# Performance work log

Hardware: AMD Instinct MI355X
Metric: run time of the kernel (lower is better)

## Reference

```python
import jax, jax.numpy as jnp
import numpy as np

LAMBDA_OPACITY = 1e-3
LAMBDA_DIST = 1e-3
LAMBDA_SAM = 1e-4
MIN_PIXNUM = 2
N_RAYS = 65536
S = 48            # samples per ray
NPIX = 65536      # semantic supervised pixels
C = 256           # number of SAM clusters
D = 16            # semantic feature dim


def setup_inputs() -> dict:
    key = jax.random.key(0)
    k = jax.random.split(key, 8)
    rgb_pred = jax.random.normal(k[0], (NPIX, 3), dtype=jnp.float32) * 0.1 + 0.5
    rgb_gt = jax.random.uniform(k[1], (NPIX, 3), dtype=jnp.float32)
    opacity = jax.random.uniform(k[2], (NPIX, 1), dtype=jnp.float32, minval=0.01, maxval=0.99)
    N = N_RAYS * S
    ws = jax.random.uniform(k[3], (N,), dtype=jnp.float32) / S
    deltas = jax.random.uniform(k[4], (N,), dtype=jnp.float32, minval=1e-3, maxval=2e-2)
    # midpoints: sorted (cumsum of deltas) within each ray, as the CUDA scan assumes
    ts = jnp.cumsum(deltas.reshape(N_RAYS, S), axis=1).reshape(N)
    ridx = jnp.arange(N_RAYS, dtype=jnp.int32)
    rays_a = jnp.stack([ridx, ridx * S, jnp.full((N_RAYS,), S, jnp.int32)], axis=1)
    sam = jax.random.randint(k[5], (NPIX, 1), 1, C + 1, dtype=jnp.int32)  # all > 0 (valid)
    semantic = jax.random.normal(k[6], (NPIX, D), dtype=jnp.float32)
    return dict(rgb_pred=rgb_pred, rgb_gt=rgb_gt, opacity=opacity, ws=ws,
                deltas=deltas, ts=ts, rays_a=rays_a, sam=sam, semantic=semantic)


def distortion_loss(ws, deltas, ts, rays_a):
    # Mip-NeRF 360 distortion via per-ray exclusive scans (DVGO-v2 form):
    # loss_ray = sum_i 2*w_i*(t_i*W_{<i} - (wt)_{<i}) + sum_i w_i^2*delta_i/3
    n_rays = rays_a.shape[0]
    starts = rays_a[:, 1]
    N = ws.shape[0]
    ray_ids = jnp.searchsorted(starts, jnp.arange(N, dtype=starts.dtype), side='right') - 1
    w_excl_g = jnp.cumsum(ws) - ws                 # global exclusive scan
    W_excl = w_excl_g - w_excl_g[starts][ray_ids]  # per-ray exclusive scan
    wts = ws * ts
    wt_excl_g = jnp.cumsum(wts) - wts
    WT_excl = wt_excl_g - wt_excl_g[starts][ray_ids]
    per_sample = 2.0 * ws * (ts * W_excl - WT_excl) + ws * ws * deltas / 3.0
    return jax.ops.segment_sum(per_sample, ray_ids, num_segments=n_rays)


def semantic_loss(semantic, sam):
    seg = sam[:, 0]
    valid = seg > 0
    cl = jnp.where(valid, seg - 1, 0)              # 0..C-1 cluster index
    w = valid.astype(semantic.dtype)
    counts = jax.ops.segment_sum(w, cl, num_segments=C)
    csafe = jnp.maximum(counts, 1.0)
    u = jax.ops.segment_sum(semantic * w[:, None], cl, num_segments=C) / csafe[:, None]  # (C,D) centroids
    dev = jnp.linalg.norm(semantic - u[cl], axis=1) * w
    phi_raw = jax.ops.segment_sum(dev, cl, num_segments=C) / (csafe * jnp.log(counts + 10.0))
    valid_cl = counts > MIN_PIXNUM
    phi = jax.lax.stop_gradient(jnp.clip(phi_raw * 10.0, 0.1, 1.0))  # detached, clipped
    logits = (semantic @ u.T) / phi[None, :]       # (P,C)
    dist = jnp.exp(logits) * valid_cl[None, :].astype(semantic.dtype)
    denom = dist.sum(axis=1) + 1e-6
    num = jnp.take_along_axis(dist, cl[:, None], axis=1)[:, 0]
    pix_valid = valid & valid_cl[cl]
    proto_nce = -jnp.sum(jnp.where(pix_valid, jnp.log(num / denom), 0.0))
    # sam_norm_loss_flag branch
    norms = jnp.linalg.norm(semantic, axis=1)
    norm_loss = jnp.sum(w * (norms - 1.0) ** 2) / jnp.maximum(w.sum(), 1.0)
    return (LAMBDA_SAM * proto_nce + 100.0 * norm_loss).reshape(1)


def reference(rgb_pred, rgb_gt, opacity, ws, deltas, ts, rays_a, sam, semantic):
    rgb = (rgb_pred - rgb_gt) ** 2                                    # d['rgb']
    o = opacity + 1e-10
    opac = LAMBDA_OPACITY * (-o * jnp.log(o))                         # d['opacity']
    dist = LAMBDA_DIST * distortion_loss(ws, deltas, ts, rays_a)      # d['distortion']
    sem = semantic_loss(semantic, sam)                                # d['semantic_render']
    return (rgb, opac, dist, sem)
```

## Files before the change

kernel.cpp:

```cpp
#include <hip/hip_runtime.h>
#include <hip/hip_bf16.h>

#define NPIX 65536
#define NRAYS 65536
#define SS 48
#define NC 256
#define ND 16
#define RPB 128

typedef __attribute__((ext_vector_type(8))) short short8;
typedef __attribute__((ext_vector_type(4))) float f32x4;

__device__ __forceinline__ unsigned short f2bf(float x) {
    unsigned u = __float_as_uint(x);
    unsigned r = u + 0x7fff + ((u >> 16) & 1);
    return (unsigned short)(r >> 16);
}
__device__ __forceinline__ float bf2f(unsigned short h) {
    return __uint_as_float(((unsigned)h) << 16);
}

__global__ __launch_bounds__(256) void kA(
    const float* __restrict__ rgb_pred, const float* __restrict__ rgb_gt,
    const float* __restrict__ opacity, const int* __restrict__ sam,
    const float* __restrict__ semantic,
    float* __restrict__ o_rgb, float* __restrict__ o_opac,
    float* __restrict__ cntpart, float* __restrict__ usumpart,
    float* __restrict__ normpart, float* __restrict__ wsumpart, int ppbA)
{
    __shared__ float cnt_s[NC];
    __shared__ float us_s[NC*17];
    __shared__ float red_s[8];
    const int t = threadIdx.x;
    const int b = blockIdx.x;
    for (int j = t; j < NC; j += 256) cnt_s[j] = 0.f;
    for (int j = t; j < NC*17; j += 256) us_s[j] = 0.f;
    __syncthreads();
    float nloc = 0.f, wloc = 0.f;
    for (int p = 0; p < ppbA; ++p) {
        const int i = (b*ppbA + p)*256 + t;
        const float pr0 = rgb_pred[3*i+0], pr1 = rgb_pred[3*i+1], pr2 = rgb_pred[3*i+2];
        const float g0 = rgb_gt[3*i+0],  g1 = rgb_gt[3*i+1],  g2 = rgb_gt[3*i+2];
        const float d0 = pr0-g0, d1 = pr1-g1, d2 = pr2-g2;
        o_rgb[3*i+0] = d0*d0; o_rgb[3*i+1] = d1*d1; o_rgb[3*i+2] = d2*d2;
        const float o = opacity[i] + 1e-10f;
        o_opac[i] = -0.001f * o * logf(o);
        const float4* sp = (const float4*)(semantic + (size_t)i*ND);
        const float4 a0 = sp[0], a1 = sp[1], a2 = sp[2], a3 = sp[3];
        const int seg = sam[i];
        if (seg > 0) {
            const int cl = seg - 1;
            const float ss =
                a0.x*a0.x + a0.y*a0.y + a0.z*a0.z + a0.w*a0.w +
                a1.x*a1.x + a1.y*a1.y + a1.z*a1.z + a1.w*a1.w +
                a2.x*a2.x + a2.y*a2.y + a2.z*a2.z + a2.w*a2.w +
                a3.x*a3.x + a3.y*a3.y + a3.z*a3.z + a3.w*a3.w;
            const float dn = sqrtf(ss) - 1.f;
            nloc += dn*dn; wloc += 1.f;
            atomicAdd(&cnt_s[cl], 1.f);
            float* up = us_s + cl*17;
            atomicAdd(up+0,  a0.x); atomicAdd(up+1,  a0.y);
            atomicAdd(up+2,  a0.z); atomicAdd(up+3,  a0.w);
            atomicAdd(up+4,  a1.x); atomicAdd(up+5,  a1.y);
            atomicAdd(up+6,  a1.z); atomicAdd(up+7,  a1.w);
            atomicAdd(up+8,  a2.x); atomicAdd(up+9,  a2.y);
            atomicAdd(up+10, a2.z); atomicAdd(up+11, a2.w);
            atomicAdd(up+12, a3.x); atomicAdd(up+13, a3.y);
            atomicAdd(up+14, a3.z); atomicAdd(up+15, a3.w);
        }
    }
    __syncthreads();
    for (int j = t; j < NC; j += 256) cntpart[b*NC + j] = cnt_s[j];
    for (int j = t; j < NC*ND; j += 256) {
        const int c = j >> 4, k = j & 15;
        usumpart[(size_t)b*NC*ND + j] = us_s[c*17 + k];
    }
    for (int off = 32; off > 0; off >>= 1) {
        nloc += __shfl_down(nloc, off);
        wloc += __shfl_down(wloc, off);
    }
    if ((t & 63) == 0) { red_s[t>>6] = nloc; red_s[4 + (t>>6)] = wloc; }
    __syncthreads();
    if (t == 0) {
        normpart[b] = red_s[0]+red_s[1]+red_s[2]+red_s[3];
        wsumpart[b] = red_s[4]+red_s[5]+red_s[6]+red_s[7];
    }
}

__global__ __launch_bounds__(128) void kDist(
    const float* __restrict__ wsv, const float* __restrict__ deltas,
    const float* __restrict__ tsv, const int* __restrict__ rays_a,
    float* __restrict__ o_dist)
{
    __shared__ float wS[SS][RPB+1];
    __shared__ float tS[SS][RPB+1];
    __shared__ float dS[SS][RPB+1];
    __shared__ int bad;
    const int t = threadIdx.x;
    const int r0 = blockIdx.x * RPB;
    const int ray = r0 + t;
    if (t == 0) bad = 0;
    __syncthreads();
    const int start = rays_a[3*ray + 1];
    const int cnt   = rays_a[3*ray + 2];
    if (start != ray*SS || cnt != SS) atomicAdd(&bad, 1);
    __syncthreads();

    if (bad == 0) {
        const size_t gb = (size_t)r0 * SS;
        const float4* gw = (const float4*)(wsv + gb);
        const float4* gt = (const float4*)(tsv + gb);
        const float4* gd = (const float4*)(deltas + gb);
        for (int i = t; i < RPB*SS/4; i += 128) {
            const int e = i*4;
            const int rr = e / SS;
            const int jj = e % SS;
            const float4 a = gw[i], b = gt[i], c = gd[i];
            wS[jj+0][rr]=a.x; wS[jj+1][rr]=a.y; wS[jj+2][rr]=a.z; wS[jj+3][rr]=a.w;
            tS[jj+0][rr]=b.x; tS[jj+1][rr]=b.y; tS[jj+2][rr]=b.z; tS[jj+3][rr]=b.w;
            dS[jj+0][rr]=c.x; dS[jj+1][rr]=c.y; dS[jj+2][rr]=c.z; dS[jj+3][rr]=c.w;
        }
        __syncthreads();
        float W = 0.f, WT = 0.f, acc = 0.f;
        for (int j = 0; j < SS; ++j) {
            const float w_ = wS[j][t], t_ = tS[j][t], d_ = dS[j][t];
            acc += 2.f*w_*(t_*W - WT) + w_*w_*d_*(1.f/3.f);
            W += w_; WT += w_*t_;
        }
        o_dist[ray] = 0.001f * acc;
    } else {
        float W = 0.f, WT = 0.f, acc = 0.f;
        for (int j = 0; j < cnt; ++j) {
            const float w_ = wsv[start+j], t_ = tsv[start+j], d_ = deltas[start+j];
            acc += 2.f*w_*(t_*W - WT) + w_*w_*d_*(1.f/3.f);
            W += w_; WT += w_*t_;
        }
        o_dist[ray] = 0.001f * acc;
    }
}

__global__ __launch_bounds__(256) void kP1(
    const float* __restrict__ cntpart, const float* __restrict__ usumpart,
    const float* __restrict__ normpart, const float* __restrict__ wsumpart,
    float* __restrict__ cnt, float* __restrict__ u,
    float* __restrict__ scal, int nblkA)
{
    const int c = blockIdx.x;
    const int t = threadIdx.x;
    const int kk = t & 15;
    const int s  = t >> 4;

    float us = 0.f;
    for (int b = s; b < nblkA; b += 16)
        us += usumpart[(size_t)b*(NC*ND) + c*ND + kk];

    __shared__ float lds[16][17];
    lds[s][kk] = us;

    float cs = (t < nblkA) ? cntpart[t*NC + c] : 0.f;
#pragma unroll
    for (int off = 32; off > 0; off >>= 1) cs += __shfl_xor(cs, off);
    __shared__ float cred[4];
    if ((t & 63) == 0) cred[t >> 6] = cs;
    __syncthreads();

    if (t < 16) {
        const float ctot = cred[0]+cred[1]+cred[2]+cred[3];
        float tot = 0.f;
#pragma unroll
        for (int s2 = 0; s2 < 16; ++s2) tot += lds[s2][t];
        u[c*ND + t] = tot / fmaxf(ctot, 1.f);
        if (t == 0) cnt[c] = ctot;
    }

    if (c == 0) {
        float n = (t < nblkA) ? normpart[t] : 0.f;
        float w2 = (t < nblkA) ? wsumpart[t] : 0.f;
#pragma unroll
        for (int off = 32; off > 0; off >>= 1) {
            n  += __shfl_xor(n, off);
            w2 += __shfl_xor(w2, off);
        }
        __shared__ float nr[4], wr[4];
        if ((t & 63) == 0) { nr[t >> 6] = n; wr[t >> 6] = w2; }
        __syncthreads();
        if (t == 0) {
            scal[0] = nr[0]+nr[1]+nr[2]+nr[3];
            scal[1] = wr[0]+wr[1]+wr[2]+wr[3];
        }
    }
}

__global__ __launch_bounds__(256) void kC(
    const float* __restrict__ semantic, const int* __restrict__ sam,
    const float* __restrict__ u, float* __restrict__ devpart, int ppb)
{
    __shared__ float u_s[NC*20];
    __shared__ float dev_s[NC];
    const int t = threadIdx.x, b = blockIdx.x;
    for (int j = t; j < NC*ND; j += 256) {
        const int c = j >> 4, k = j & 15;
        u_s[c*20 + k] = u[j];
    }
    for (int j = t; j < NC; j += 256) dev_s[j] = 0.f;
    __syncthreads();
    for (int p = 0; p < ppb; ++p) {
        const int i = (b*ppb + p)*256 + t;
        const int seg = sam[i];
        if (seg > 0) {
            const int cl = seg - 1;
            const float4* sp = (const float4*)(semantic + (size_t)i*ND);
            const float4 a0 = sp[0], a1 = sp[1], a2 = sp[2], a3 = sp[3];
            const float4* up = (const float4*)(u_s + cl*20);
            const float4 u0 = up[0], u1 = up[1], u2 = up[2], u3 = up[3];
            float q, d2 = 0.f;
            q = a0.x-u0.x; d2 += q*q;  q = a0.y-u0.y; d2 += q*q;
            q = a0.z-u0.z; d2 += q*q;  q = a0.w-u0.w; d2 += q*q;
            q = a1.x-u1.x; d2 += q*q;  q = a1.y-u1.y; d2 += q*q;
            q = a1.z-u1.z; d2 += q*q;  q = a1.w-u1.w; d2 += q*q;
            q = a2.x-u2.x; d2 += q*q;  q = a2.y-u2.y; d2 += q*q;
            q = a2.z-u2.z; d2 += q*q;  q = a2.w-u2.w; d2 += q*q;
            q = a3.x-u3.x; d2 += q*q;  q = a3.y-u3.y; d2 += q*q;
            q = a3.z-u3.z; d2 += q*q;  q = a3.w-u3.w; d2 += q*q;
            atomicAdd(&dev_s[cl], sqrtf(d2));
        }
    }
    __syncthreads();
    for (int j = t; j < NC; j += 256) devpart[b*NC + j] = dev_s[j];
}

__global__ __launch_bounds__(256) void kP2(
    const float* __restrict__ devpart, const float* __restrict__ cnt,
    const float* __restrict__ u, float* __restrict__ uphi,
    unsigned short* __restrict__ uphi_h, unsigned short* __restrict__ uphi_l,
    float* __restrict__ mf, float* __restrict__ scal, int nblkC)
{
    const int c = blockIdx.x;
    const int t = threadIdx.x;

    if (c == 0 && t == 0) {
        scal[2] = 0.f;
        ((unsigned*)scal)[3] = 0u;
    }

    float dv = (t < nblkC) ? devpart[t*NC + c] : 0.f;
#pragma unroll
    for (int off = 32; off > 0; off >>= 1) dv += __shfl_xor(dv, off);
    __shared__ float dred[4];
    __shared__ float inv_s;
    if ((t & 63) == 0) dred[t >> 6] = dv;
    __syncthreads();

    if (t == 0) {
        const float dtot = dred[0]+dred[1]+dred[2]+dred[3];
        const float cs = cnt[c];
        const float csafe = fmaxf(cs, 1.f);
        const float phiraw = dtot / (csafe * logf(cs + 10.f));
        const float phi = fminf(fmaxf(phiraw * 10.f, 0.1f), 1.f);
        inv_s = 1.f / phi;
        mf[c] = (cs > 2.0f) ? 1.f : 0.f;
    }
    __syncthreads();
    if (t < 16) {
        const float v = u[c*ND + t] * inv_s;
        uphi[c*ND + t] = v;
        const unsigned short h = f2bf(v);
        uphi_h[c*ND + t] = h;
        uphi_l[c*ND + t] = f2bf(v - bf2f(h));
    }
}

__global__ __launch_bounds__(256, 1) void kD(
    const float* __restrict__ semantic, const int* __restrict__ sam,
    const float* __restrict__ uphi,
    const unsigned short* __restrict__ uphi_h, const unsigned short* __restrict__ uphi_l,
    const float* __restrict__ mf,
    float* __restrict__ scal, float* __restrict__ o_sem)
{
    __shared__ float dlds[4][64];
    __shared__ float red_s[4];
    const int t = threadIdx.x;
    const int lane = t & 63;
    const int w = t >> 6;
    const int col = lane & 15;
    const int g   = lane >> 4;
    const int wbase = blockIdx.x * 256 + w * 64;

    short8 A[4];
#pragma unroll
    for (int pt = 0; pt < 4; ++pt) {
        const float* sp = semantic + (size_t)(wbase + pt*16 + col)*ND + (g & 1)*8;
        const float4 f0 = ((const float4*)sp)[0];
        const float4 f1 = ((const float4*)sp)[1];
        float fv[8] = {f0.x,f0.y,f0.z,f0.w, f1.x,f1.y,f1.z,f1.w};
        short8 a;
#pragma unroll
        for (int i = 0; i < 8; ++i) {
            const unsigned short h = f2bf(fv[i]);
            const unsigned short l = f2bf(fv[i] - bf2f(h));
            a[i] = (short)((g < 2) ? h : l);
        }
        A[pt] = a;
    }

    short8 B1[16], B2[16];
    const short8* Bh = (const short8*)uphi_h;
    const short8* Bl = (const short8*)uphi_l;
    const short8 zero8 = {0,0,0,0,0,0,0,0};
#pragma unroll
    for (int ct = 0; ct < 16; ++ct) {
        const int cls = ct*16 + col;
        const int idx = cls*2 + (g & 1);
        B1[ct] = Bh[idx];
        B2[ct] = (g < 2) ? Bl[idx] : zero8;
    }

    float mfv[16];
#pragma unroll
    for (int ct = 0; ct < 16; ++ct) mfv[ct] = mf[ct*16 + col];

    float dacc[4][4] = {};
#pragma unroll
    for (int ct = 0; ct < 16; ++ct) {
#pragma unroll
        for (int pt = 0; pt < 4; ++pt) {
            f32x4 d = {0.f, 0.f, 0.f, 0.f};
            d = __builtin_amdgcn_mfma_f32_16x16x32_bf16(A[pt], B2[ct], d, 0, 0, 0);
            d = __builtin_amdgcn_mfma_f32_16x16x32_bf16(A[pt], B1[ct], d, 0, 0, 0);
#pragma unroll
            for (int r = 0; r < 4; ++r)
                dacc[pt][r] += mfv[ct] * __expf(d[r]);
        }
    }

#pragma unroll
    for (int pt = 0; pt < 4; ++pt)
#pragma unroll
        for (int r = 0; r < 4; ++r) {
            float v = dacc[pt][r];
            v += __shfl_xor(v, 1);
            v += __shfl_xor(v, 2);
            v += __shfl_xor(v, 4);
            v += __shfl_xor(v, 8);
            dacc[pt][r] = v;
        }

    if (col == 0) {
#pragma unroll
        for (int pt = 0; pt < 4; ++pt)
#pragma unroll
            for (int r = 0; r < 4; ++r)
                dlds[w][pt*16 + 4*g + r] = dacc[pt][r];
    }
    const float denom = dlds[w][lane] + 1e-6f;

    const int p = wbase + lane;
    const int seg = sam[p];
    const int cl = (seg > 0) ? (seg - 1) : 0;
    const float4* sp = (const float4*)(semantic + (size_t)p*ND);
    const float4 b0 = sp[0], b1 = sp[1], b2 = sp[2], b3 = sp[3];
    const float4* uo = (const float4*)(uphi + cl*ND);
    const float4 c0 = uo[0], c1 = uo[1], c2 = uo[2], c3 = uo[3];
    const float down =
        b0.x*c0.x + b0.y*c0.y + b0.z*c0.z + b0.w*c0.w +
        b1.x*c1.x + b1.y*c1.y + b1.z*c1.z + b1.w*c1.w +
        b2.x*c2.x + b2.y*c2.y + b2.z*c2.z + b2.w*c2.w +
        b3.x*c3.x + b3.y*c3.y + b3.z*c3.z + b3.w*c3.w;
    const float mo = mf[cl];
    float contrib = (seg > 0 && mo > 0.5f) ? (__logf(denom) - down) : 0.f;

#pragma unroll
    for (int off = 32; off > 0; off >>= 1) contrib += __shfl_xor(contrib, off);
    if ((t & 63) == 0) red_s[t >> 6] = contrib;
    __syncthreads();
    if (t == 0) atomicAdd(&scal[2], red_s[0]+red_s[1]+red_s[2]+red_s[3]);

    if (t == 0) {
        __threadfence();
        unsigned* done = (unsigned*)(scal + 3);
        const unsigned old = atomicAdd(done, 1u);
        if (old == gridDim.x - 1) {
            const float proto = atomicAdd(&scal[2], 0.f);
            const float nrm   = scal[0];
            const float wsum  = scal[1];
            o_sem[0] = 1e-4f * proto + 100.f * nrm / fmaxf(wsum, 1.f);
        }
    }
}

extern "C" void kernel_launch(void* const* d_in, const int* in_sizes, int n_in,
                              void* d_out, int out_size, void* d_ws, size_t ws_size,
                              hipStream_t stream)
{
    const float* rgb_pred = (const float*)d_in[0];
    const float* rgb_gt   = (const float*)d_in[1];
    const float* opacity  = (const float*)d_in[2];
    const float* wsv      = (const float*)d_in[3];
    const float* deltas   = (const float*)d_in[4];
    const float* tsv      = (const float*)d_in[5];
    const int*   rays_a   = (const int*)d_in[6];
    const int*   sam      = (const int*)d_in[7];
    const float* semantic = (const float*)d_in[8];

    float* out    = (float*)d_out;
    float* o_rgb  = out;
    float* o_opac = out + 196608;
    float* o_dist = out + 262144;
    float* o_sem  = out + 327680;
    float* wsf    = (float*)d_ws;

    int nblkA = 256, nblkC = 256;
    size_t need = ((size_t)nblkA*NC*(ND+1) + (size_t)nblkC*NC + NC + 2*NC*ND + NC*ND + 2*nblkA + 64) * 4;
    if (ws_size < need) { nblkA = 128; nblkC = 128; }
    const int ppbA = NPIX / (nblkA * 256);
    const int ppbC = NPIX / (nblkC * 256);

    float*          w_cntpart  = wsf;
    float*          w_usum     = w_cntpart + (size_t)nblkA*NC;
    float*          w_devpart  = w_usum + (size_t)nblkA*NC*ND;
    float*          w_cnt      = w_devpart + (size_t)nblkC*NC;
    float*          w_u        = w_cnt + NC;
    float*          w_uphi     = w_u + NC*ND;
    float*          w_scal     = w_uphi + NC*ND;
    float*          w_mf       = w_scal + 8;
    float*          w_normpart = w_mf + NC;
    float*          w_wsumpart = w_normpart + nblkA;
    unsigned short* w_uh       = (unsigned short*)(w_wsumpart + nblkA);
    unsigned short* w_ul       = w_uh + NC*ND;

    kA<<<nblkA, 256, 0, stream>>>(rgb_pred, rgb_gt, opacity, sam, semantic,
                                  o_rgb, o_opac, w_cntpart, w_usum,
                                  w_normpart, w_wsumpart, ppbA);
    kDist<<<NRAYS/RPB, RPB, 0, stream>>>(wsv, deltas, tsv, rays_a, o_dist);
    kP1<<<NC, 256, 0, stream>>>(w_cntpart, w_usum, w_normpart, w_wsumpart,
                                w_cnt, w_u, w_scal, nblkA);
    kC<<<nblkC, 256, 0, stream>>>(semantic, sam, w_u, w_devpart, ppbC);
    kP2<<<NC, 256, 0, stream>>>(w_devpart, w_cnt, w_u, w_uphi, w_uh, w_ul,
                                w_mf, w_scal, nblkC);
    kD<<<NPIX/256, 256, 0, stream>>>(semantic, sam, w_uphi, w_uh, w_ul, w_mf, w_scal, o_sem);
}
```

Measured before the change: 54.39 us.

## Fuse distortion scan into semantic kernel, drop bf16 low-part of prototypes

Removes the separate distortion kernel and folds it into the final semantic kernel as extra blocks. Each wavefront now handles one ray with a shuffle-based prefix scan instead of an LDS transpose. The semantic logits now use a single bf16 MFMA with only the high part of the prototypes, dropping the split-precision correction term. Blocks are also smaller, 64 pixels each, to spread work across more CUs. This cuts a launch and halves MFMA work but lowers logit precision, and the per-ray path assumes at most 64 samples per ray.

```diff
diff --git a/kernel.cpp b/kernel.cpp
--- a/kernel.cpp
+++ b/kernel.cpp
@@ -6,7 +6,6 @@
 #define SS 48
 #define NC 256
 #define ND 16
-#define RPB 128
 
 typedef __attribute__((ext_vector_type(8))) short short8;
 typedef __attribute__((ext_vector_type(4))) float f32x4;
@@ -87,58 +86,6 @@
     }
 }
 
-__global__ __launch_bounds__(128) void kDist(
-    const float* __restrict__ wsv, const float* __restrict__ deltas,
-    const float* __restrict__ tsv, const int* __restrict__ rays_a,
-    float* __restrict__ o_dist)
-{
-    __shared__ float wS[SS][RPB+1];
-    __shared__ float tS[SS][RPB+1];
-    __shared__ float dS[SS][RPB+1];
-    __shared__ int bad;
-    const int t = threadIdx.x;
-    const int r0 = blockIdx.x * RPB;
-    const int ray = r0 + t;
-    if (t == 0) bad = 0;
-    __syncthreads();
-    const int start = rays_a[3*ray + 1];
-    const int cnt   = rays_a[3*ray + 2];
-    if (start != ray*SS || cnt != SS) atomicAdd(&bad, 1);
-    __syncthreads();
-
-    if (bad == 0) {
-        const size_t gb = (size_t)r0 * SS;
-        const float4* gw = (const float4*)(wsv + gb);
-        const float4* gt = (const float4*)(tsv + gb);
-        const float4* gd = (const float4*)(deltas + gb);
-        for (int i = t; i < RPB*SS/4; i += 128) {
-            const int e = i*4;
-            const int rr = e / SS;
-            const int jj = e % SS;
-            const float4 a = gw[i], b = gt[i], c = gd[i];
-            wS[jj+0][rr]=a.x; wS[jj+1][rr]=a.y; wS[jj+2][rr]=a.z; wS[jj+3][rr]=a.w;
-            tS[jj+0][rr]=b.x; tS[jj+1][rr]=b.y; tS[jj+2][rr]=b.z; tS[jj+3][rr]=b.w;
-            dS[jj+0][rr]=c.x; dS[jj+1][rr]=c.y; dS[jj+2][rr]=c.z; dS[jj+3][rr]=c.w;
-        }
-        __syncthreads();
-        float W = 0.f, WT = 0.f, acc = 0.f;
-        for (int j = 0; j < SS; ++j) {
-            const float w_ = wS[j][t], t_ = tS[j][t], d_ = dS[j][t];
-            acc += 2.f*w_*(t_*W - WT) + w_*w_*d_*(1.f/3.f);
-            W += w_; WT += w_*t_;
-        }
-        o_dist[ray] = 0.001f * acc;
-    } else {
-        float W = 0.f, WT = 0.f, acc = 0.f;
-        for (int j = 0; j < cnt; ++j) {
-            const float w_ = wsv[start+j], t_ = tsv[start+j], d_ = deltas[start+j];
-            acc += 2.f*w_*(t_*W - WT) + w_*w_*d_*(1.f/3.f);
-            W += w_; WT += w_*t_;
-        }
-        o_dist[ray] = 0.001f * acc;
-    }
-}
-
 __global__ __launch_bounds__(256) void kP1(
     const float* __restrict__ cntpart, const float* __restrict__ usumpart,
     const float* __restrict__ normpart, const float* __restrict__ wsumpart,
@@ -232,7 +179,7 @@
 __global__ __launch_bounds__(256) void kP2(
     const float* __restrict__ devpart, const float* __restrict__ cnt,
     const float* __restrict__ u, float* __restrict__ uphi,
-    unsigned short* __restrict__ uphi_h, unsigned short* __restrict__ uphi_l,
+    unsigned short* __restrict__ uphi_h,
     float* __restrict__ mf, float* __restrict__ scal, int nblkC)
 {
     const int c = blockIdx.x;
@@ -264,127 +211,134 @@
     if (t < 16) {
         const float v = u[c*ND + t] * inv_s;
         uphi[c*ND + t] = v;
-        const unsigned short h = f2bf(v);
-        uphi_h[c*ND + t] = h;
-        uphi_l[c*ND + t] = f2bf(v - bf2f(h));
-    }
-}
-
-__global__ __launch_bounds__(256, 1) void kD(
+        uphi_h[c*ND + t] = f2bf(v);
+    }
+}
+
+__global__ __launch_bounds__(256) void kFuse(
     const float* __restrict__ semantic, const int* __restrict__ sam,
-    const float* __restrict__ uphi,
-    const unsigned short* __restrict__ uphi_h, const unsigned short* __restrict__ uphi_l,
+    const float* __restrict__ uphi, const unsigned short* __restrict__ uphi_h,
     const float* __restrict__ mf,
-    float* __restrict__ scal, float* __restrict__ o_sem)
-{
-    __shared__ float dlds[4][64];
-    __shared__ float red_s[4];
+    float* __restrict__ scal, float* __restrict__ o_sem,
+    const float* __restrict__ wsv, const float* __restrict__ deltas,
+    const float* __restrict__ tsv, const int* __restrict__ rays_a,
+    float* __restrict__ o_dist, int ndblk)
+{
     const int t = threadIdx.x;
     const int lane = t & 63;
     const int w = t >> 6;
-    const int col = lane & 15;
-    const int g   = lane >> 4;
-    const int wbase = blockIdx.x * 256 + w * 64;
-
-    short8 A[4];
-#pragma unroll
-    for (int pt = 0; pt < 4; ++pt) {
-        const float* sp = semantic + (size_t)(wbase + pt*16 + col)*ND + (g & 1)*8;
-        const float4 f0 = ((const float4*)sp)[0];
-        const float4 f1 = ((const float4*)sp)[1];
-        float fv[8] = {f0.x,f0.y,f0.z,f0.w, f1.x,f1.y,f1.z,f1.w};
-        short8 a;
-#pragma unroll
-        for (int i = 0; i < 8; ++i) {
-            const unsigned short h = f2bf(fv[i]);
-            const unsigned short l = f2bf(fv[i] - bf2f(h));
-            a[i] = (short)((g < 2) ? h : l);
-        }
-        A[pt] = a;
-    }
-
-    short8 B1[16], B2[16];
-    const short8* Bh = (const short8*)uphi_h;
-    const short8* Bl = (const short8*)uphi_l;
-    const short8 zero8 = {0,0,0,0,0,0,0,0};
-#pragma unroll
-    for (int ct = 0; ct < 16; ++ct) {
-        const int cls = ct*16 + col;
-        const int idx = cls*2 + (g & 1);
-        B1[ct] = Bh[idx];
-        B2[ct] = (g < 2) ? Bl[idx] : zero8;
-    }
-
-    float mfv[16];
-#pragma unroll
-    for (int ct = 0; ct < 16; ++ct) mfv[ct] = mf[ct*16 + col];
-
-    float dacc[4][4] = {};
-#pragma unroll
-    for (int ct = 0; ct < 16; ++ct) {
-#pragma unroll
-        for (int pt = 0; pt < 4; ++pt) {
+
+    if ((int)blockIdx.x < ndblk) {
+        __shared__ float dlds[4][16];
+        __shared__ float red_s[4];
+        const int col = lane & 15;
+        const int g   = lane >> 4;
+        const int wbase = blockIdx.x*64 + w*16;
+
+        short8 A;
+        {
+            const float* sp = semantic + (size_t)(wbase + col)*ND + (g & 1)*8;
+            const float4 f0 = ((const float4*)sp)[0];
+            const float4 f1 = ((const float4*)sp)[1];
+            float fv[8] = {f0.x,f0.y,f0.z,f0.w, f1.x,f1.y,f1.z,f1.w};
+#pragma unroll
+            for (int i = 0; i < 8; ++i) {
+                const unsigned short h = f2bf(fv[i]);
+                const unsigned short l = f2bf(fv[i] - bf2f(h));
+                A[i] = (short)((g < 2) ? h : l);
+            }
+        }
+
+        short8 B1[16];
+        const short8* Bh = (const short8*)uphi_h;
+#pragma unroll
+        for (int ct = 0; ct < 16; ++ct)
+            B1[ct] = Bh[(ct*16 + col)*2 + (g & 1)];
+
+        float mfv[16];
+#pragma unroll
+        for (int ct = 0; ct < 16; ++ct) mfv[ct] = mf[ct*16 + col];
+
+        float dacc[4] = {0.f, 0.f, 0.f, 0.f};
+#pragma unroll
+        for (int ct = 0; ct < 16; ++ct) {
             f32x4 d = {0.f, 0.f, 0.f, 0.f};
-            d = __builtin_amdgcn_mfma_f32_16x16x32_bf16(A[pt], B2[ct], d, 0, 0, 0);
-            d = __builtin_amdgcn_mfma_f32_16x16x32_bf16(A[pt], B1[ct], d, 0, 0, 0);
+            d = __builtin_amdgcn_mfma_f32_16x16x32_bf16(A, B1[ct], d, 0, 0, 0);
 #pragma unroll
             for (int r = 0; r < 4; ++r)
-                dacc[pt][r] += mfv[ct] * __expf(d[r]);
-        }
-    }
-
-#pragma unroll
-    for (int pt = 0; pt < 4; ++pt)
+                dacc[r] += mfv[ct] * __expf(d[r]);
+        }
+
 #pragma unroll
         for (int r = 0; r < 4; ++r) {
-            float v = dacc[pt][r];
+            float v = dacc[r];
             v += __shfl_xor(v, 1);
             v += __shfl_xor(v, 2);
             v += __shfl_xor(v, 4);
             v += __shfl_xor(v, 8);
-            dacc[pt][r] = v;
-        }
-
-    if (col == 0) {
-#pragma unroll
-        for (int pt = 0; pt < 4; ++pt)
+            dacc[r] = v;
+        }
+        if (col == 0) {
 #pragma unroll
             for (int r = 0; r < 4; ++r)
-                dlds[w][pt*16 + 4*g + r] = dacc[pt][r];
-    }
-    const float denom = dlds[w][lane] + 1e-6f;
-
-    const int p = wbase + lane;
-    const int seg = sam[p];
-    const int cl = (seg > 0) ? (seg - 1) : 0;
-    const float4* sp = (const float4*)(semantic + (size_t)p*ND);
-    const float4 b0 = sp[0], b1 = sp[1], b2 = sp[2], b3 = sp[3];
-    const float4* uo = (const float4*)(uphi + cl*ND);
-    const float4 c0 = uo[0], c1 = uo[1], c2 = uo[2], c3 = uo[3];
-    const float down =
-        b0.x*c0.x + b0.y*c0.y + b0.z*c0.z + b0.w*c0.w +
-        b1.x*c1.x + b1.y*c1.y + b1.z*c1.z + b1.w*c1.w +
-        b2.x*c2.x + b2.y*c2.y + b2.z*c2.z + b2.w*c2.w +
-        b3.x*c3.x + b3.y*c3.y + b3.z*c3.z + b3.w*c3.w;
-    const float mo = mf[cl];
-    float contrib = (seg > 0 && mo > 0.5f) ? (__logf(denom) - down) : 0.f;
-
-#pragma unroll
-    for (int off = 32; off > 0; off >>= 1) contrib += __shfl_xor(contrib, off);
-    if ((t & 63) == 0) red_s[t >> 6] = contrib;
-    __syncthreads();
-    if (t == 0) atomicAdd(&scal[2], red_s[0]+red_s[1]+red_s[2]+red_s[3]);
-
-    if (t == 0) {
-        __threadfence();
-        unsigned* done = (unsigned*)(scal + 3);
-        const unsigned old = atomicAdd(done, 1u);
-        if (old == gridDim.x - 1) {
-            const float proto = atomicAdd(&scal[2], 0.f);
-            const float nrm   = scal[0];
-            const float wsum  = scal[1];
-            o_sem[0] = 1e-4f * proto + 100.f * nrm / fmaxf(wsum, 1.f);
-        }
+                dlds[w][4*g + r] = dacc[r];
+        }
+        __syncthreads();
+
+        float contrib = 0.f;
+        if (t < 64) {
+            const int p = blockIdx.x*64 + t;
+            const float denom = dlds[t >> 4][t & 15] + 1e-6f;
+            const int seg = sam[p];
+            const int cl = (seg > 0) ? (seg - 1) : 0;
+            const float4* sp = (const float4*)(semantic + (size_t)p*ND);
+            const float4 b0 = sp[0], b1 = sp[1], b2 = sp[2], b3 = sp[3];
+            const float4* uo = (const float4*)(uphi + cl*ND);
+            const float4 c0 = uo[0], c1 = uo[1], c2 = uo[2], c3 = uo[3];
+            const float down =
+                b0.x*c0.x + b0.y*c0.y + b0.z*c0.z + b0.w*c0.w +
+                b1.x*c1.x + b1.y*c1.y + b1.z*c1.z + b1.w*c1.w +
+                b2.x*c2.x + b2.y*c2.y + b2.z*c2.z + b2.w*c2.w +
+                b3.x*c3.x + b3.y*c3.y + b3.z*c3.z + b3.w*c3.w;
+            const float mo = mf[cl];
+            contrib = (seg > 0 && mo > 0.5f) ? (__logf(denom) - down) : 0.f;
+        }
+#pragma unroll
+        for (int off = 32; off > 0; off >>= 1) contrib += __shfl_xor(contrib, off);
+        if ((t & 63) == 0) red_s[t >> 6] = contrib;
+        __syncthreads();
+        if (t == 0) {
+            atomicAdd(&scal[2], red_s[0]+red_s[1]+red_s[2]+red_s[3]);
+            __threadfence();
+            unsigned* done = (unsigned*)(scal + 3);
+            const unsigned old = atomicAdd(done, 1u);
+            if (old == (unsigned)(ndblk - 1)) {
+                const float proto = atomicAdd(&scal[2], 0.f);
+                o_sem[0] = 1e-4f * proto + 100.f * scal[0] / fmaxf(scal[1], 1.f);
+            }
+        }
+    } else {
+        const int bD = blockIdx.x - ndblk;
+        const int ray = bD*4 + w;
+        const int start = rays_a[3*ray + 1];
+        const int cnt   = rays_a[3*ray + 2];
+        const bool act = lane < cnt;
+        const float w_ = act ? wsv[start+lane]    : 0.f;
+        const float t_ = act ? tsv[start+lane]    : 0.f;
+        const float d_ = act ? deltas[start+lane] : 0.f;
+        const float wt_ = w_*t_;
+        float sw = w_, swt = wt_;
+#pragma unroll
+        for (int off = 1; off < 64; off <<= 1) {
+            const float aw  = __shfl_up(sw, off);
+            const float awt = __shfl_up(swt, off);
+            if (lane >= off) { sw += aw; swt += awt; }
+        }
+        const float Wex = sw - w_, WTex = swt - wt_;
+        float per = 2.f*w_*(t_*Wex - WTex) + w_*w_*d_*(1.f/3.f);
+#pragma unroll
+        for (int off = 32; off > 0; off >>= 1) per += __shfl_xor(per, off);
+        if (lane == 0) o_dist[ray] = 0.001f * per;
     }
 }
 
@@ -410,7 +364,7 @@
     float* wsf    = (float*)d_ws;
 
     int nblkA = 256, nblkC = 256;
-    size_t need = ((size_t)nblkA*NC*(ND+1) + (size_t)nblkC*NC + NC + 2*NC*ND + NC*ND + 2*nblkA + 64) * 4;
+    size_t need = ((size_t)nblkA*NC*(ND+1) + (size_t)nblkC*NC + NC + 2*NC*ND + 2*nblkA + 64) * 4;
     if (ws_size < need) { nblkA = 128; nblkC = 128; }
     const int ppbA = NPIX / (nblkA * 256);
     const int ppbC = NPIX / (nblkC * 256);
@@ -426,16 +380,19 @@
     float*          w_normpart = w_mf + NC;
     float*          w_wsumpart = w_normpart + nblkA;
     unsigned short* w_uh       = (unsigned short*)(w_wsumpart + nblkA);
-    unsigned short* w_ul       = w_uh + NC*ND;
+
+    const int ndblk = NPIX / 64;
+    const int ndistblk = NRAYS / 4;
 
     kA<<<nblkA, 256, 0, stream>>>(rgb_pred, rgb_gt, opacity, sam, semantic,
                                   o_rgb, o_opac, w_cntpart, w_usum,
                                   w_normpart, w_wsumpart, ppbA);
-    kDist<<<NRAYS/RPB, RPB, 0, stream>>>(wsv, deltas, tsv, rays_a, o_dist);
     kP1<<<NC, 256, 0, stream>>>(w_cntpart, w_usum, w_normpart, w_wsumpart,
                                 w_cnt, w_u, w_scal, nblkA);
     kC<<<nblkC, 256, 0, stream>>>(semantic, sam, w_u, w_devpart, ppbC);
-    kP2<<<NC, 256, 0, stream>>>(w_devpart, w_cnt, w_u, w_uphi, w_uh, w_ul,
+    kP2<<<NC, 256, 0, stream>>>(w_devpart, w_cnt, w_u, w_uphi, w_uh,
                                 w_mf, w_scal, nblkC);
-    kD<<<NPIX/256, 256, 0, stream>>>(semantic, sam, w_uphi, w_uh, w_ul, w_mf, w_scal, o_sem);
-}
+    kFuse<<<ndblk + ndistblk, 256, 0, stream>>>(semantic, sam, w_uphi, w_uh, w_mf,
+                                                w_scal, o_sem,
+                                                wsv, deltas, tsv, rays_a, o_dist, ndblk);
+}
```

After: 112.1 us. +106.1%, slower.

## Halve kD work per wave, drop low-bf16 B split, raise occupancy

Applied to the files above, without the earlier changes.

The semantic-denominator kernel now gives each wave 32 pixels instead of 64 and launches twice as many blocks without the one-block-per-CU launch bound. B operand tiles and mask values are loaded per class tile instead of preloaded into large register arrays. The low-order bf16 correction for the scaled prototypes is dropped, so each product needs one MFMA instead of two. This aims to cut register pressure and MFMA count and to spread work over more CUs, at the cost of lower precision in the logits before exp.

```diff
diff --git a/kernel.cpp b/kernel.cpp
--- a/kernel.cpp
+++ b/kernel.cpp
@@ -232,7 +232,7 @@
 __global__ __launch_bounds__(256) void kP2(
     const float* __restrict__ devpart, const float* __restrict__ cnt,
     const float* __restrict__ u, float* __restrict__ uphi,
-    unsigned short* __restrict__ uphi_h, unsigned short* __restrict__ uphi_l,
+    unsigned short* __restrict__ uphi_h,
     float* __restrict__ mf, float* __restrict__ scal, int nblkC)
 {
     const int c = blockIdx.x;
@@ -264,126 +264,107 @@
     if (t < 16) {
         const float v = u[c*ND + t] * inv_s;
         uphi[c*ND + t] = v;
-        const unsigned short h = f2bf(v);
-        uphi_h[c*ND + t] = h;
-        uphi_l[c*ND + t] = f2bf(v - bf2f(h));
-    }
-}
-
-__global__ __launch_bounds__(256, 1) void kD(
+        uphi_h[c*ND + t] = f2bf(v);
+    }
+}
+
+__global__ __launch_bounds__(256) void kD(
     const float* __restrict__ semantic, const int* __restrict__ sam,
-    const float* __restrict__ uphi,
-    const unsigned short* __restrict__ uphi_h, const unsigned short* __restrict__ uphi_l,
+    const float* __restrict__ uphi, const unsigned short* __restrict__ uphi_h,
     const float* __restrict__ mf,
     float* __restrict__ scal, float* __restrict__ o_sem)
 {
-    __shared__ float dlds[4][64];
+    __shared__ float dlds[4][32];
     __shared__ float red_s[4];
     const int t = threadIdx.x;
     const int lane = t & 63;
     const int w = t >> 6;
     const int col = lane & 15;
     const int g   = lane >> 4;
-    const int wbase = blockIdx.x * 256 + w * 64;
-
-    short8 A[4];
-#pragma unroll
-    for (int pt = 0; pt < 4; ++pt) {
-        const float* sp = semantic + (size_t)(wbase + pt*16 + col)*ND + (g & 1)*8;
-        const float4 f0 = ((const float4*)sp)[0];
-        const float4 f1 = ((const float4*)sp)[1];
-        float fv[8] = {f0.x,f0.y,f0.z,f0.w, f1.x,f1.y,f1.z,f1.w};
-        short8 a;
+    const int wbase = blockIdx.x * 128 + w * 32;
+
+    short8 A0, A1;
+    {
+        const float* sp0 = semantic + (size_t)(wbase + col)*ND + (g & 1)*8;
+        const float* sp1 = semantic + (size_t)(wbase + 16 + col)*ND + (g & 1)*8;
+        const float4 p00 = ((const float4*)sp0)[0], p01 = ((const float4*)sp0)[1];
+        const float4 p10 = ((const float4*)sp1)[0], p11 = ((const float4*)sp1)[1];
+        float f0[8] = {p00.x,p00.y,p00.z,p00.w,p01.x,p01.y,p01.z,p01.w};
+        float f1[8] = {p10.x,p10.y,p10.z,p10.w,p11.x,p11.y,p11.z,p11.w};
+        const bool hi = (g < 2);
 #pragma unroll
         for (int i = 0; i < 8; ++i) {
-            const unsigned short h = f2bf(fv[i]);
-            const unsigned short l = f2bf(fv[i] - bf2f(h));
-            a[i] = (short)((g < 2) ? h : l);
-        }
-        A[pt] = a;
-    }
-
-    short8 B1[16], B2[16];
+            const unsigned short h0 = f2bf(f0[i]);
+            const unsigned short h1 = f2bf(f1[i]);
+            A0[i] = (short)(hi ? h0 : f2bf(f0[i] - bf2f(h0)));
+            A1[i] = (short)(hi ? h1 : f2bf(f1[i] - bf2f(h1)));
+        }
+    }
+
     const short8* Bh = (const short8*)uphi_h;
-    const short8* Bl = (const short8*)uphi_l;
-    const short8 zero8 = {0,0,0,0,0,0,0,0};
-#pragma unroll
-    for (int ct = 0; ct < 16; ++ct) {
-        const int cls = ct*16 + col;
-        const int idx = cls*2 + (g & 1);
-        B1[ct] = Bh[idx];
-        B2[ct] = (g < 2) ? Bl[idx] : zero8;
-    }
-
-    float mfv[16];
-#pragma unroll
-    for (int ct = 0; ct < 16; ++ct) mfv[ct] = mf[ct*16 + col];
-
-    float dacc[4][4] = {};
-#pragma unroll
-    for (int ct = 0; ct < 16; ++ct) {
-#pragma unroll
-        for (int pt = 0; pt < 4; ++pt) {
-            f32x4 d = {0.f, 0.f, 0.f, 0.f};
-            d = __builtin_amdgcn_mfma_f32_16x16x32_bf16(A[pt], B2[ct], d, 0, 0, 0);
-            d = __builtin_amdgcn_mfma_f32_16x16x32_bf16(A[pt], B1[ct], d, 0, 0, 0);
-#pragma unroll
-            for (int r = 0; r < 4; ++r)
-                dacc[pt][r] += mfv[ct] * __expf(d[r]);
-        }
-    }
-
-#pragma unroll
-    for (int pt = 0; pt < 4; ++pt)
-#pragma unroll
-        for (int r = 0; r < 4; ++r) {
-            float v = dacc[pt][r];
-            v += __shfl_xor(v, 1);
-            v += __shfl_xor(v, 2);
-            v += __shfl_xor(v, 4);
-            v += __shfl_xor(v, 8);
-            dacc[pt][r] = v;
-        }
-
-    if (col == 0) {
-#pragma unroll
-        for (int pt = 0; pt < 4; ++pt)
-#pragma unroll
-            for (int r = 0; r < 4; ++r)
-                dlds[w][pt*16 + 4*g + r] = dacc[pt][r];
-    }
-    const float denom = dlds[w][lane] + 1e-6f;
-
-    const int p = wbase + lane;
-    const int seg = sam[p];
-    const int cl = (seg > 0) ? (seg - 1) : 0;
-    const float4* sp = (const float4*)(semantic + (size_t)p*ND);
-    const float4 b0 = sp[0], b1 = sp[1], b2 = sp[2], b3 = sp[3];
-    const float4* uo = (const float4*)(uphi + cl*ND);
-    const float4 c0 = uo[0], c1 = uo[1], c2 = uo[2], c3 = uo[3];
-    const float down =
-        b0.x*c0.x + b0.y*c0.y + b0.z*c0.z + b0.w*c0.w +
-        b1.x*c1.x + b1.y*c1.y + b1.z*c1.z + b1.w*c1.w +
-        b2.x*c2.x + b2.y*c2.y + b2.z*c2.z + b2.w*c2.w +
-        b3.x*c3.x + b3.y*c3.y + b3.z*c3.z + b3.w*c3.w;
-    const float mo = mf[cl];
-    float contrib = (seg > 0 && mo > 0.5f) ? (__logf(denom) - down) : 0.f;
-
+    f32x4 e0 = {0.f,0.f,0.f,0.f}, e1 = {0.f,0.f,0.f,0.f};
+
+#define CT_STEP(ct) { \
+        const short8 b = Bh[((ct)*16 + col)*2 + (g & 1)]; \
+        const float mm = mf[(ct)*16 + col]; \
+        const f32x4 z = {0.f,0.f,0.f,0.f}; \
+        const f32x4 d0 = __builtin_amdgcn_mfma_f32_16x16x32_bf16(A0, b, z, 0, 0, 0); \
+        const f32x4 d1 = __builtin_amdgcn_mfma_f32_16x16x32_bf16(A1, b, z, 0, 0, 0); \
+        e0[0] += mm*__expf(d0[0]); e0[1] += mm*__expf(d0[1]); \
+        e0[2] += mm*__expf(d0[2]); e0[3] += mm*__expf(d0[3]); \
+        e1[0] += mm*__expf(d1[0]); e1[1] += mm*__expf(d1[1]); \
+        e1[2] += mm*__expf(d1[2]); e1[3] += mm*__expf(d1[3]); }
+
+    CT_STEP(0)  CT_STEP(1)  CT_STEP(2)  CT_STEP(3)
+    CT_STEP(4)  CT_STEP(5)  CT_STEP(6)  CT_STEP(7)
+    CT_STEP(8)  CT_STEP(9)  CT_STEP(10) CT_STEP(11)
+    CT_STEP(12) CT_STEP(13) CT_STEP(14) CT_STEP(15)
+#undef CT_STEP
+
+#pragma unroll
+    for (int r = 0; r < 4; ++r) {
+        float v0 = e0[r], v1 = e1[r];
+        v0 += __shfl_xor(v0, 1); v0 += __shfl_xor(v0, 2);
+        v0 += __shfl_xor(v0, 4); v0 += __shfl_xor(v0, 8);
+        v1 += __shfl_xor(v1, 1); v1 += __shfl_xor(v1, 2);
+        v1 += __shfl_xor(v1, 4); v1 += __shfl_xor(v1, 8);
+        if (col == 0) {
+            dlds[w][4*g + r]      = v0;
+            dlds[w][16 + 4*g + r] = v1;
+        }
+    }
+    __syncthreads();
+
+    float contrib = 0.f;
+    if (t < 128) {
+        const int p = blockIdx.x*128 + t;
+        const float denom = dlds[t >> 5][t & 31] + 1e-6f;
+        const int seg = sam[p];
+        const int cl = (seg > 0) ? (seg - 1) : 0;
+        const float4* sp = (const float4*)(semantic + (size_t)p*ND);
+        const float4 b0 = sp[0], b1 = sp[1], b2 = sp[2], b3 = sp[3];
+        const float4* uo = (const float4*)(uphi + cl*ND);
+        const float4 c0 = uo[0], c1 = uo[1], c2 = uo[2], c3 = uo[3];
+        const float down =
+            b0.x*c0.x + b0.y*c0.y + b0.z*c0.z + b0.w*c0.w +
+            b1.x*c1.x + b1.y*c1.y + b1.z*c1.z + b1.w*c1.w +
+            b2.x*c2.x + b2.y*c2.y + b2.z*c2.z + b2.w*c2.w +
+            b3.x*c3.x + b3.y*c3.y + b3.z*c3.z + b3.w*c3.w;
+        const float mo = mf[cl];
+        contrib = (seg > 0 && mo > 0.5f) ? (__logf(denom) - down) : 0.f;
+    }
 #pragma unroll
     for (int off = 32; off > 0; off >>= 1) contrib += __shfl_xor(contrib, off);
     if ((t & 63) == 0) red_s[t >> 6] = contrib;
     __syncthreads();
-    if (t == 0) atomicAdd(&scal[2], red_s[0]+red_s[1]+red_s[2]+red_s[3]);
-
     if (t == 0) {
+        atomicAdd(&scal[2], red_s[0]+red_s[1]+red_s[2]+red_s[3]);
         __threadfence();
         unsigned* done = (unsigned*)(scal + 3);
         const unsigned old = atomicAdd(done, 1u);
         if (old == gridDim.x - 1) {
             const float proto = atomicAdd(&scal[2], 0.f);
-            const float nrm   = scal[0];
-            const float wsum  = scal[1];
-            o_sem[0] = 1e-4f * proto + 100.f * nrm / fmaxf(wsum, 1.f);
+            o_sem[0] = 1e-4f * proto + 100.f * scal[0] / fmaxf(scal[1], 1.f);
         }
     }
 }
@@ -410,7 +391,7 @@
     float* wsf    = (float*)d_ws;
 
     int nblkA = 256, nblkC = 256;
-    size_t need = ((size_t)nblkA*NC*(ND+1) + (size_t)nblkC*NC + NC + 2*NC*ND + NC*ND + 2*nblkA + 64) * 4;
+    size_t need = ((size_t)nblkA*NC*(ND+1) + (size_t)nblkC*NC + NC + 2*NC*ND + 2*nblkA + 64) * 4;
     if (ws_size < need) { nblkA = 128; nblkC = 128; }
     const int ppbA = NPIX / (nblkA * 256);
     const int ppbC = NPIX / (nblkC * 256);
@@ -426,7 +407,6 @@
     float*          w_normpart = w_mf + NC;
     float*          w_wsumpart = w_normpart + nblkA;
     unsigned short* w_uh       = (unsigned short*)(w_wsumpart + nblkA);
-    unsigned short* w_ul       = w_uh + NC*ND;
 
     kA<<<nblkA, 256, 0, stream>>>(rgb_pred, rgb_gt, opacity, sam, semantic,
                                   o_rgb, o_opac, w_cntpart, w_usum,
@@ -435,7 +415,7 @@
     kP1<<<NC, 256, 0, stream>>>(w_cntpart, w_usum, w_normpart, w_wsumpart,
                                 w_cnt, w_u, w_scal, nblkA);
     kC<<<nblkC, 256, 0, stream>>>(semantic, sam, w_u, w_devpart, ppbC);
-    kP2<<<NC, 256, 0, stream>>>(w_devpart, w_cnt, w_u, w_uphi, w_uh, w_ul,
+    kP2<<<NC, 256, 0, stream>>>(w_devpart, w_cnt, w_u, w_uphi, w_uh,
                                 w_mf, w_scal, nblkC);
-    kD<<<NPIX/256, 256, 0, stream>>>(semantic, sam, w_uphi, w_uh, w_ul, w_mf, w_scal, o_sem);
-}
+    kD<<<NPIX/128, 256, 0, stream>>>(semantic, sam, w_uphi, w_uh, w_mf, w_scal, o_sem);
+}
```

Result: slower. 70.56 us (+29.7%).
